# Kernel optimization log

Hardware: AMD Instinct MI355X
Metric: run time of the kernel (lower is better)

Reference implementation:

```python
import jax, jax.numpy as jnp
import numpy as np
from jax import lax

B, T, S, H, E, V = 32, 64, 64, 512, 512, 32000


def setup_inputs() -> dict:
    key = jax.random.key(0)
    ks = jax.random.split(key, 10)
    s = 0.02
    return {
        "sequence": jax.random.randint(ks[0], (B, T), 0, V),
        "encoder_outputs": jax.random.normal(ks[1], (S, B, H), jnp.float32),
        "encoder_hidden": jax.random.normal(ks[2], (B, H), jnp.float32),
        "encoder_cell": jax.random.normal(ks[3], (B, H), jnp.float32),
        "embedding": jax.random.normal(ks[4], (V, E), jnp.float32) * s,
        "W_ih": jax.random.normal(ks[5], (4 * H, E + H), jnp.float32) * s,
        "b_ih": jnp.zeros((4 * H,), jnp.float32),
        "W_hh": jax.random.normal(ks[6], (4 * H, H), jnp.float32) * s,
        "b_hh": jnp.zeros((4 * H,), jnp.float32),
        "W_in_proj": jax.random.normal(ks[7], (H, H), jnp.float32) * s,
        "b_in_proj": jnp.zeros((H,), jnp.float32),
        "W_out_proj": jax.random.normal(ks[8], (H, 2 * H), jnp.float32) * s,
        "b_out_proj": jnp.zeros((H,), jnp.float32),
        "W_final": jax.random.normal(ks[9], (V, H), jnp.float32) * s,
        "b_final": jnp.zeros((V,), jnp.float32),
    }


def reference(sequence, encoder_outputs, encoder_hidden, encoder_cell,
              embedding, W_ih, b_ih, W_hh, b_hh,
              W_in_proj, b_in_proj, W_out_proj, b_out_proj,
              W_final, b_final):
    # embed: [B,T,E] -> [T,B,E] (dropout_in = 0 -> identity)
    x = embedding[sequence].transpose(1, 0, 2)
    input_feed = jnp.zeros((B, H), x.dtype)

    def step(carry, x_t):
        h, c, feed = carry
        inp = jnp.concatenate([x_t, feed], axis=1)          # [B, E+H]
        gates = inp @ W_ih.T + b_ih + h @ W_hh.T + b_hh     # [B, 4H]
        i, f, g, o = jnp.split(gates, 4, axis=1)
        c = jax.nn.sigmoid(f) * c + jax.nn.sigmoid(i) * jnp.tanh(g)
        h = jax.nn.sigmoid(o) * jnp.tanh(c)
        # attention layer (scores computed but unused downstream, as in source)
        xp = h @ W_in_proj.T + b_in_proj                    # [B, H]
        scores = jax.nn.softmax(
            jnp.einsum('sbh,bh->sb', encoder_outputs, xp), axis=0)  # [S, B]
        out = jnp.tanh(jnp.concatenate([xp, h], axis=1) @ W_out_proj.T + b_out_proj)
        return (h, c, out), (out, scores)

    _, (outs, _attn) = lax.scan(step, (encoder_hidden, encoder_cell, input_feed), x)
    # outs: [T,B,H] -> [B,T,H] -> logits [B,T,V]
    logits = outs.transpose(1, 0, 2) @ W_final.T + b_final
    return logits
```

## Files before the change

### kernel.cpp

```cpp
#include <hip/hip_runtime.h>
#include <hip/hip_bf16.h>

#define BB 32
#define TT 64
#define HH 512
#define EE 512
#define VV 32000

typedef float f32x4 __attribute__((ext_vector_type(4)));
typedef float f32x16 __attribute__((ext_vector_type(16)));
typedef __bf16 bf16x8 __attribute__((ext_vector_type(8)));
typedef unsigned short u16x8 __attribute__((ext_vector_type(8)));

static __device__ __forceinline__ unsigned short f2bf(float f) {
  unsigned int u = __builtin_bit_cast(unsigned int, f);
  u += 0x7fffu + ((u >> 16) & 1u);
  return (unsigned short)(u >> 16);
}

__global__ __launch_bounds__(256) void k_cvt_bf16(const float* __restrict__ in,
                                                  unsigned short* __restrict__ out,
                                                  int n8) {
  int tid = blockIdx.x * 256 + threadIdx.x;
  if (tid >= n8) return;
  int idx = tid * 8;
  float4 a = *(const float4*)(in + idx);
  float4 b = *(const float4*)(in + idx + 4);
  u16x8 o;
  o[0] = f2bf(a.x); o[1] = f2bf(a.y); o[2] = f2bf(a.z); o[3] = f2bf(a.w);
  o[4] = f2bf(b.x); o[5] = f2bf(b.y); o[6] = f2bf(b.z); o[7] = f2bf(b.w);
  *(u16x8*)(out + idx) = o;
}

__global__ __launch_bounds__(256) void k_emb(const int* __restrict__ seq,
                                             const float* __restrict__ emb,
                                             unsigned short* __restrict__ out) {
  int tid = blockIdx.x * 256 + threadIdx.x;
  int idx = tid * 8;
  int m = idx >> 9;
  int e0 = idx & 511;
  int t = m >> 5, b = m & 31;
  int s = seq[b * TT + t];
  const float* src = emb + (size_t)s * EE + e0;
  float4 a = *(const float4*)(src);
  float4 c = *(const float4*)(src + 4);
  u16x8 o;
  o[0] = f2bf(a.x); o[1] = f2bf(a.y); o[2] = f2bf(a.z); o[3] = f2bf(a.w);
  o[4] = f2bf(c.x); o[5] = f2bf(c.y); o[6] = f2bf(c.z); o[7] = f2bf(c.w);
  *(u16x8*)(out + m * EE + e0) = o;
}

__global__ __launch_bounds__(256) void k_weff(const float* __restrict__ W_out,
                                              const float* __restrict__ W_in,
                                              float* __restrict__ W_eff) {
  __shared__ float sa[16][17], sb[16][17];
  const int t16 = threadIdx.x & 15, ty = threadIdx.x >> 4;
  const int i = blockIdx.y * 16 + ty, m = blockIdx.x * 16 + t16;
  float acc = 0.f;
  for (int k0 = 0; k0 < HH; k0 += 16) {
    sa[ty][t16] = W_out[i * 1024 + k0 + t16];
    sb[ty][t16] = W_in[(k0 + ty) * HH + m];
    __syncthreads();
#pragma unroll
    for (int kk = 0; kk < 16; ++kk) acc += sa[ty][kk] * sb[kk][t16];
    __syncthreads();
  }
  W_eff[i * HH + m] = acc + W_out[i * 1024 + HH + m];
}

__global__ __launch_bounds__(256) void k_beff(const float* __restrict__ W_out,
                                              const float* __restrict__ b_in,
                                              const float* __restrict__ b_out,
                                              float* __restrict__ b_eff) {
  int i = blockIdx.x * 256 + threadIdx.x;
  if (i >= HH) return;
  float acc = b_out[i];
  for (int k = 0; k < HH; ++k) acc += W_out[i * 1024 + k] * b_in[k];
  b_eff[i] = acc;
}

__global__ __launch_bounds__(256) void k_gemm(const unsigned short* __restrict__ A, int lda,
                                              const unsigned short* __restrict__ Bm, int ldb,
                                              float* __restrict__ C, int ldc,
                                              const float* __restrict__ bias1,
                                              const float* __restrict__ bias2,
                                              const float* __restrict__ biasR1,
                                              const float* __restrict__ biasR2,
                                              int K, int m_panels) {
  __shared__ unsigned short As[128][40];
  __shared__ unsigned short Bs[128][40];
  const int tx = threadIdx.x;
  const int lane = tx & 63, w = tx >> 6;
  const int wrow = (w >> 1) * 64, wcol = (w & 1) * 64;
  const int l15 = lane & 15, lk = lane >> 4;
  const int nb = gridDim.x;
  const int swz = (blockIdx.x & 7) * (nb >> 3) + (blockIdx.x >> 3);
  const int m0 = (swz % m_panels) * 128, n0 = (swz / m_panels) * 128;
  f32x4 acc[4][4] = {};
  for (int k0 = 0; k0 < K; k0 += 32) {
#pragma unroll
    for (int u = 0; u < 2; ++u) {
      int c = u * 256 + tx;
      int row = c >> 2, cc = (c & 3) * 8;
      *(int4*)(&As[row][cc]) = *(const int4*)(A + (size_t)(m0 + row) * lda + k0 + cc);
      *(int4*)(&Bs[row][cc]) = *(const int4*)(Bm + (size_t)(n0 + row) * ldb + k0 + cc);
    }
    __syncthreads();
    bf16x8 av[4], bv[4];
#pragma unroll
    for (int mi = 0; mi < 4; ++mi)
      av[mi] = __builtin_bit_cast(bf16x8, *(const int4*)(&As[wrow + mi * 16 + l15][lk * 8]));
#pragma unroll
    for (int ni = 0; ni < 4; ++ni)
      bv[ni] = __builtin_bit_cast(bf16x8, *(const int4*)(&Bs[wcol + ni * 16 + l15][lk * 8]));
#pragma unroll
    for (int mi = 0; mi < 4; ++mi)
#pragma unroll
      for (int ni = 0; ni < 4; ++ni)
        acc[mi][ni] = __builtin_amdgcn_mfma_f32_16x16x32_bf16(av[mi], bv[ni], acc[mi][ni], 0, 0, 0);
    __syncthreads();
  }
#pragma unroll
  for (int mi = 0; mi < 4; ++mi) {
#pragma unroll
    for (int ni = 0; ni < 4; ++ni) {
      int row = m0 + wrow + mi * 16 + lk * 4;
      int col = n0 + wcol + ni * 16 + l15;
      float bb = 0.f;
      if (bias1) bb += bias1[col];
      if (bias2) bb += bias2[col];
#pragma unroll
      for (int q = 0; q < 4; ++q) {
        float bR = 0.f;
        if (biasR1) bR += biasR1[row + q];
        if (biasR2) bR += biasR2[row + q];
        C[(size_t)(row + q) * ldc + col] = acc[mi][ni][q] + bb + bR;
      }
    }
  }
}

static __device__ __forceinline__ void gbar(unsigned* __restrict__ bar, unsigned gen) {
  __syncthreads();
  if (threadIdx.x == 0) {
    asm volatile("s_waitcnt vmcnt(0)" ::: "memory");
    __hip_atomic_store(&bar[blockIdx.x], gen, __ATOMIC_RELAXED, __HIP_MEMORY_SCOPE_AGENT);
  }
  if (threadIdx.x < 64) {
    while (__hip_atomic_load(&bar[threadIdx.x], __ATOMIC_RELAXED, __HIP_MEMORY_SCOPE_AGENT) < gen)
      __builtin_amdgcn_s_sleep(1);
  }
  __syncthreads();
  asm volatile("" ::: "memory");
}

__global__ __launch_bounds__(256, 1) void k_recur(
    const float* __restrict__ xprojT,
    const unsigned short* __restrict__ wih_b,
    const unsigned short* __restrict__ whh_b,
    const unsigned short* __restrict__ weff_b,
    const float* __restrict__ b_eff,
    const float* __restrict__ enc_c,
    unsigned short* __restrict__ h_ext,
    unsigned short* __restrict__ outs_ext,
    unsigned* __restrict__ bar)
{
  __shared__ int4 Abuf4[4096];
  __shared__ float red[4][32][32];
  char* Abuf = (char*)Abuf4;

  const int tx = threadIdx.x;
  const int bid = blockIdx.x;
  const int i0 = bid * 8;
  const int w = tx >> 6, l = tx & 63;
  const int jl = l & 31;
  const int kh = (l >> 5) * 8;
  const int u = tx >> 5, b = tx & 31;

  bf16x8 wg[16];
  {
    const int jg = (jl >> 3) * 512 + i0 + (jl & 7);
#pragma unroll
    for (int r = 0; r < 16; ++r) {
      int k0 = (w * 16 + r) * 16 + kh;
      const unsigned short* src = (k0 < 512)
          ? wih_b + (size_t)jg * 1024 + 512 + k0
          : whh_b + (size_t)jg * 512 + (k0 - 512);
      wg[r] = __builtin_bit_cast(bf16x8, *(const int4*)src);
    }
  }
  bf16x8 we[8];
  {
    const int wr = (bid >> 2) * 32 + jl;
#pragma unroll
    for (int r = 0; r < 8; ++r) {
      int k0 = (w * 8 + r) * 16 + kh;
      we[r] = __builtin_bit_cast(bf16x8, *(const int4*)(weff_b + (size_t)wr * 512 + k0));
    }
  }
  float c_reg = enc_c[b * 512 + i0 + u];
  const float be = b_eff[i0 + u];

  auto stage = [&](const unsigned short* __restrict__ src, int half) {
#pragma unroll
    for (int rnd = 0; rnd < 8; ++rnd) {
      int id = rnd * 256 + tx;
      int row = id >> 6, c16 = id & 63;
      int4 v = *(const int4*)(src + (size_t)row * 512 + c16 * 8);
      int byte = (row * 2048 + half * 1024 + c16 * 16) ^ ((row & 7) << 4);
      *(int4*)(Abuf + byte) = v;
    }
  };
  auto afrag = [&](int ktile) -> bf16x8 {
    int byte = (jl * 2048 + ktile * 32 + (l >> 5) * 16) ^ ((jl & 7) << 4);
    return __builtin_bit_cast(bf16x8, *(const int4*)(Abuf + byte));
  };

  stage(outs_ext, 0);
  stage(h_ext, 1);
  __syncthreads();

  unsigned gen = 1;
  for (int t = 0; t < 64; ++t) {
    f32x16 acc = {};
#pragma unroll
    for (int r = 0; r < 16; ++r)
      acc = __builtin_amdgcn_mfma_f32_32x32x16_bf16(wg[r], afrag(w * 16 + r), acc, 0, 0, 0);
#pragma unroll
    for (int reg = 0; reg < 16; ++reg) {
      int row = (reg & 3) + 8 * (reg >> 2) + 4 * (l >> 5);
      red[w][row][jl] = acc[reg];
    }
    __syncthreads();
    {
      float g4[4];
#pragma unroll
      for (int g = 0; g < 4; ++g) {
        float s = red[0][g * 8 + u][b] + red[1][g * 8 + u][b]
                + red[2][g * 8 + u][b] + red[3][g * 8 + u][b];
        s += xprojT[(size_t)(g * 512 + i0 + u) * 2048 + t * 32 + b];
        g4[g] = s;
      }
      float si = 1.f / (1.f + __expf(-g4[0]));
      float sf = 1.f / (1.f + __expf(-g4[1]));
      float so = 1.f / (1.f + __expf(-g4[3]));
      float cn = sf * c_reg + si * tanhf(g4[2]);
      c_reg = cn;
      unsigned hb = f2bf(so * tanhf(cn));
      unsigned other = (unsigned)__shfl_down((int)hb, 32);
      if ((u & 1) == 0) {
        unsigned* h32 = (unsigned*)(h_ext + (size_t)(t + 1) * 16384);
        __hip_atomic_store(&h32[b * 256 + bid * 4 + (u >> 1)], hb | (other << 16),
                           __ATOMIC_RELAXED, __HIP_MEMORY_SCOPE_AGENT);
      }
    }
    gbar(bar, gen++);

    stage(h_ext + (size_t)(t + 1) * 16384, 1);
    __syncthreads();
    f32x16 acc2 = {};
#pragma unroll
    for (int r = 0; r < 8; ++r)
      acc2 = __builtin_amdgcn_mfma_f32_32x32x16_bf16(we[r], afrag(32 + w * 8 + r), acc2, 0, 0, 0);
#pragma unroll
    for (int reg = 0; reg < 16; ++reg) {
      int row = (reg & 3) + 8 * (reg >> 2) + 4 * (l >> 5);
      red[w][row][jl] = acc2[reg];
    }
    __syncthreads();
    {
      int row = (bid & 3) * 8 + u;
      float s = red[0][row][b] + red[1][row][b] + red[2][row][b] + red[3][row][b] + be;
      unsigned ob = f2bf(tanhf(s));
      unsigned other = (unsigned)__shfl_down((int)ob, 32);
      if ((u & 1) == 0) {
        unsigned* o32 = (unsigned*)(outs_ext + (size_t)(t + 1) * 16384);
        __hip_atomic_store(&o32[b * 256 + bid * 4 + (u >> 1)], ob | (other << 16),
                           __ATOMIC_RELAXED, __HIP_MEMORY_SCOPE_AGENT);
      }
    }
    gbar(bar, gen++);

    if (t < 63) {
      stage(outs_ext + (size_t)(t + 1) * 16384, 0);
      __syncthreads();
    }
  }
}

__global__ __launch_bounds__(256) void k_tr(const unsigned short* __restrict__ outs,
                                            unsigned short* __restrict__ abt) {
  int tid = blockIdx.x * 256 + threadIdx.x;
  int idx = tid * 8;
  int m = idx >> 9;
  int h0 = idx & 511;
  int b = m >> 6, t = m & 63;
  *(u16x8*)(abt + m * 512 + h0) =
      *(const u16x8*)(outs + (size_t)(t * 32 + b) * 512 + h0);
}

extern "C" void kernel_launch(void* const* d_in, const int* in_sizes, int n_in,
                              void* d_out, int out_size, void* d_ws, size_t ws_size,
                              hipStream_t stream) {
  const int*   seq      = (const int*)d_in[0];
  const float* enc_h    = (const float*)d_in[2];
  const float* enc_c    = (const float*)d_in[3];
  const float* emb      = (const float*)d_in[4];
  const float* W_ih     = (const float*)d_in[5];
  const float* b_ih     = (const float*)d_in[6];
  const float* W_hh     = (const float*)d_in[7];
  const float* b_hh     = (const float*)d_in[8];
  const float* W_inp    = (const float*)d_in[9];
  const float* b_inp    = (const float*)d_in[10];
  const float* W_outp   = (const float*)d_in[11];
  const float* b_outp   = (const float*)d_in[12];
  const float* W_final  = (const float*)d_in[13];
  const float* b_final  = (const float*)d_in[14];
  float* logits = (float*)d_out;

  char* ws = (char*)d_ws;
  size_t off = 0;
  auto alloc = [&](size_t bytes) {
    char* p = ws + off;
    off += (bytes + 255) & ~(size_t)255;
    return p;
  };
  unsigned short* wih_b  = (unsigned short*)alloc((size_t)2048 * 1024 * 2);
  unsigned short* whh_b  = (unsigned short*)alloc((size_t)2048 * 512 * 2);
  unsigned short* wfin_b = (unsigned short*)alloc((size_t)VV * HH * 2);
  unsigned short* weff_b = (unsigned short*)alloc((size_t)512 * 512 * 2);
  unsigned short* emb_b  = (unsigned short*)alloc((size_t)2048 * 512 * 2);
  float* xprojT = (float*)alloc((size_t)2048 * 2048 * 4);
  float* W_eff  = (float*)alloc((size_t)512 * 512 * 4);
  float* b_eff  = (float*)alloc((size_t)512 * 4);
  unsigned short* h_ext  = (unsigned short*)alloc((size_t)65 * 32 * 512 * 2);
  unsigned short* outs_e = (unsigned short*)alloc((size_t)65 * 32 * 512 * 2);
  unsigned short* abt = (unsigned short*)alloc((size_t)2048 * 512 * 2);
  unsigned* bar = (unsigned*)alloc(4096);

  hipMemsetAsync(bar, 0, 4096, stream);
  hipMemsetAsync(outs_e, 0, (size_t)32 * 512 * 2, stream);

  hipLaunchKernelGGL(k_cvt_bf16, dim3(1024), dim3(256), 0, stream, W_ih, wih_b, 2048 * 1024 / 8);
  hipLaunchKernelGGL(k_cvt_bf16, dim3(512), dim3(256), 0, stream, W_hh, whh_b, 2048 * 512 / 8);
  hipLaunchKernelGGL(k_cvt_bf16, dim3(8000), dim3(256), 0, stream, W_final, wfin_b, VV * HH / 8);
  hipLaunchKernelGGL(k_cvt_bf16, dim3(8), dim3(256), 0, stream, enc_h, h_ext, 32 * 512 / 8);
  hipLaunchKernelGGL(k_emb, dim3(512), dim3(256), 0, stream, seq, emb, emb_b);
  hipLaunchKernelGGL(k_weff, dim3(32, 32), dim3(256), 0, stream, W_outp, W_inp, W_eff);
  hipLaunchKernelGGL(k_cvt_bf16, dim3(128), dim3(256), 0, stream, W_eff, weff_b, 512 * 512 / 8);
  hipLaunchKernelGGL(k_beff, dim3(2), dim3(256), 0, stream, W_outp, b_inp, b_outp, b_eff);

  hipLaunchKernelGGL(k_gemm, dim3(256), dim3(256), 0, stream,
                     wih_b, 1024, emb_b, 512, xprojT, 2048,
                     (const float*)nullptr, (const float*)nullptr, b_ih, b_hh, 512, 16);

  hipLaunchKernelGGL(k_recur, dim3(64), dim3(256), 0, stream,
                     xprojT, wih_b, whh_b, weff_b, b_eff, enc_c,
                     h_ext, outs_e, bar);

  hipLaunchKernelGGL(k_tr, dim3(512), dim3(256), 0, stream, outs_e + 16384, abt);
  hipLaunchKernelGGL(k_gemm, dim3(4000), dim3(256), 0, stream,
                     abt, 512, wfin_b, 512, logits, 32000,
                     b_final, (const float*)nullptr, (const float*)nullptr, (const float*)nullptr, 512, 16);
}
```

Before: 818.1 us.

## Fuse W_final bf16 conversion into GEMM and streamline recurrent barrier publishing

The final-logits GEMM now reads W_final as fp32 and converts it to bf16 while loading tiles, which removes the separate conversion kernel and its intermediate buffer. The recurrent kernel pads the barrier flags to separate cache lines, packs h and output values through shared memory into 64-bit atomic stores, and splits staging so each step loads only the needed half. The xproj load and feed staging are hoisted ahead of the MFMA loop to hide latency. In exchange, the big GEMM reads twice as many bytes for B and repeats the conversion for each M panel.

```diff
diff --git a/kernel.cpp b/kernel.cpp
--- a/kernel.cpp
+++ b/kernel.cpp
@@ -80,7 +80,8 @@
 }
 
 __global__ __launch_bounds__(256) void k_gemm(const unsigned short* __restrict__ A, int lda,
-                                              const unsigned short* __restrict__ Bm, int ldb,
+                                              const unsigned short* __restrict__ Bm,
+                                              const float* __restrict__ BmF, int ldb,
                                               float* __restrict__ C, int ldc,
                                               const float* __restrict__ bias1,
                                               const float* __restrict__ bias2,
@@ -103,7 +104,17 @@
       int c = u * 256 + tx;
       int row = c >> 2, cc = (c & 3) * 8;
       *(int4*)(&As[row][cc]) = *(const int4*)(A + (size_t)(m0 + row) * lda + k0 + cc);
-      *(int4*)(&Bs[row][cc]) = *(const int4*)(Bm + (size_t)(n0 + row) * ldb + k0 + cc);
+      if (BmF) {
+        const float* src = BmF + (size_t)(n0 + row) * ldb + k0 + cc;
+        float4 f0 = *(const float4*)src;
+        float4 f1 = *(const float4*)(src + 4);
+        u16x8 pk;
+        pk[0] = f2bf(f0.x); pk[1] = f2bf(f0.y); pk[2] = f2bf(f0.z); pk[3] = f2bf(f0.w);
+        pk[4] = f2bf(f1.x); pk[5] = f2bf(f1.y); pk[6] = f2bf(f1.z); pk[7] = f2bf(f1.w);
+        *(u16x8*)(&Bs[row][cc]) = pk;
+      } else {
+        *(int4*)(&Bs[row][cc]) = *(const int4*)(Bm + (size_t)(n0 + row) * ldb + k0 + cc);
+      }
     }
     __syncthreads();
     bf16x8 av[4], bv[4];
@@ -144,10 +155,10 @@
   __syncthreads();
   if (threadIdx.x == 0) {
     asm volatile("s_waitcnt vmcnt(0)" ::: "memory");
-    __hip_atomic_store(&bar[blockIdx.x], gen, __ATOMIC_RELAXED, __HIP_MEMORY_SCOPE_AGENT);
+    __hip_atomic_store(&bar[blockIdx.x * 32], gen, __ATOMIC_RELAXED, __HIP_MEMORY_SCOPE_AGENT);
   }
   if (threadIdx.x < 64) {
-    while (__hip_atomic_load(&bar[threadIdx.x], __ATOMIC_RELAXED, __HIP_MEMORY_SCOPE_AGENT) < gen)
+    while (__hip_atomic_load(&bar[threadIdx.x * 32], __ATOMIC_RELAXED, __HIP_MEMORY_SCOPE_AGENT) < gen)
       __builtin_amdgcn_s_sleep(1);
   }
   __syncthreads();
@@ -167,6 +178,7 @@
 {
   __shared__ int4 Abuf4[4096];
   __shared__ float red[4][32][32];
+  __shared__ unsigned short s_pub[32][8];
   char* Abuf = (char*)Abuf4;
 
   const int tx = threadIdx.x;
@@ -201,13 +213,23 @@
   float c_reg = enc_c[b * 512 + i0 + u];
   const float be = b_eff[i0 + u];
 
-  auto stage = [&](const unsigned short* __restrict__ src, int half) {
-#pragma unroll
-    for (int rnd = 0; rnd < 8; ++rnd) {
-      int id = rnd * 256 + tx;
-      int row = id >> 6, c16 = id & 63;
-      int4 v = *(const int4*)(src + (size_t)row * 512 + c16 * 8);
-      int byte = (row * 2048 + half * 1024 + c16 * 16) ^ ((row & 7) << 4);
+  auto stage_feed = [&](const unsigned short* __restrict__ src) {
+#pragma unroll
+    for (int r = 0; r < 16; ++r) {
+      int id = r * 64 + l;
+      int row = id >> 5, c = id & 31;
+      int4 v = *(const int4*)(src + (size_t)row * 512 + w * 256 + c * 8);
+      int byte = (row * 2048 + w * 512 + c * 16) ^ ((row & 7) << 4);
+      *(int4*)(Abuf + byte) = v;
+    }
+  };
+  auto stage_h = [&](const unsigned short* __restrict__ src) {
+#pragma unroll
+    for (int r = 0; r < 8; ++r) {
+      int id = r * 64 + l;
+      int row = id >> 4, c = id & 15;
+      int4 v = *(const int4*)(src + (size_t)row * 512 + w * 128 + c * 8);
+      int byte = (row * 2048 + 1024 + w * 256 + c * 16) ^ ((row & 7) << 4);
       *(int4*)(Abuf + byte) = v;
     }
   };
@@ -216,12 +238,16 @@
     return __builtin_bit_cast(bf16x8, *(const int4*)(Abuf + byte));
   };
 
-  stage(outs_ext, 0);
-  stage(h_ext, 1);
+  stage_h(h_ext);
   __syncthreads();
 
   unsigned gen = 1;
   for (int t = 0; t < 64; ++t) {
+    if (w < 2) stage_feed(outs_ext + (size_t)t * 16384);
+    float xp[4];
+#pragma unroll
+    for (int g = 0; g < 4; ++g)
+      xp[g] = xprojT[(size_t)(g * 512 + i0 + u) * 2048 + t * 32 + b];
     f32x16 acc = {};
 #pragma unroll
     for (int r = 0; r < 16; ++r)
@@ -235,29 +261,27 @@
     {
       float g4[4];
 #pragma unroll
-      for (int g = 0; g < 4; ++g) {
-        float s = red[0][g * 8 + u][b] + red[1][g * 8 + u][b]
-                + red[2][g * 8 + u][b] + red[3][g * 8 + u][b];
-        s += xprojT[(size_t)(g * 512 + i0 + u) * 2048 + t * 32 + b];
-        g4[g] = s;
-      }
+      for (int g = 0; g < 4; ++g)
+        g4[g] = red[0][g * 8 + u][b] + red[1][g * 8 + u][b]
+              + red[2][g * 8 + u][b] + red[3][g * 8 + u][b] + xp[g];
       float si = 1.f / (1.f + __expf(-g4[0]));
       float sf = 1.f / (1.f + __expf(-g4[1]));
       float so = 1.f / (1.f + __expf(-g4[3]));
       float cn = sf * c_reg + si * tanhf(g4[2]);
       c_reg = cn;
-      unsigned hb = f2bf(so * tanhf(cn));
-      unsigned other = (unsigned)__shfl_down((int)hb, 32);
-      if ((u & 1) == 0) {
-        unsigned* h32 = (unsigned*)(h_ext + (size_t)(t + 1) * 16384);
-        __hip_atomic_store(&h32[b * 256 + bid * 4 + (u >> 1)], hb | (other << 16),
-                           __ATOMIC_RELAXED, __HIP_MEMORY_SCOPE_AGENT);
-      }
+      s_pub[b][u] = f2bf(so * tanhf(cn));
+    }
+    __syncthreads();
+    if (tx < 64) {
+      int bb = tx & 31, half = tx >> 5;
+      unsigned long long v = *(const unsigned long long*)(&s_pub[bb][half * 4]);
+      unsigned long long* h64 = (unsigned long long*)(h_ext + (size_t)(t + 1) * 16384);
+      __hip_atomic_store(&h64[bb * 128 + bid * 2 + half], v,
+                         __ATOMIC_RELAXED, __HIP_MEMORY_SCOPE_AGENT);
     }
     gbar(bar, gen++);
 
-    stage(h_ext + (size_t)(t + 1) * 16384, 1);
-    __syncthreads();
+    stage_h(h_ext + (size_t)(t + 1) * 16384);
     f32x16 acc2 = {};
 #pragma unroll
     for (int r = 0; r < 8; ++r)
@@ -271,20 +295,17 @@
     {
       int row = (bid & 3) * 8 + u;
       float s = red[0][row][b] + red[1][row][b] + red[2][row][b] + red[3][row][b] + be;
-      unsigned ob = f2bf(tanhf(s));
-      unsigned other = (unsigned)__shfl_down((int)ob, 32);
-      if ((u & 1) == 0) {
-        unsigned* o32 = (unsigned*)(outs_ext + (size_t)(t + 1) * 16384);
-        __hip_atomic_store(&o32[b * 256 + bid * 4 + (u >> 1)], ob | (other << 16),
-                           __ATOMIC_RELAXED, __HIP_MEMORY_SCOPE_AGENT);
-      }
+      s_pub[b][u] = f2bf(tanhf(s));
+    }
+    __syncthreads();
+    if (tx < 64) {
+      int bb = tx & 31, half = tx >> 5;
+      unsigned long long v = *(const unsigned long long*)(&s_pub[bb][half * 4]);
+      unsigned long long* o64 = (unsigned long long*)(outs_ext + (size_t)(t + 1) * 16384);
+      __hip_atomic_store(&o64[bb * 128 + bid * 2 + half], v,
+                         __ATOMIC_RELAXED, __HIP_MEMORY_SCOPE_AGENT);
     }
     gbar(bar, gen++);
-
-    if (t < 63) {
-      stage(outs_ext + (size_t)(t + 1) * 16384, 0);
-      __syncthreads();
-    }
   }
 }
 
@@ -327,7 +348,6 @@
   };
   unsigned short* wih_b  = (unsigned short*)alloc((size_t)2048 * 1024 * 2);
   unsigned short* whh_b  = (unsigned short*)alloc((size_t)2048 * 512 * 2);
-  unsigned short* wfin_b = (unsigned short*)alloc((size_t)VV * HH * 2);
   unsigned short* weff_b = (unsigned short*)alloc((size_t)512 * 512 * 2);
   unsigned short* emb_b  = (unsigned short*)alloc((size_t)2048 * 512 * 2);
   float* xprojT = (float*)alloc((size_t)2048 * 2048 * 4);
@@ -336,14 +356,13 @@
   unsigned short* h_ext  = (unsigned short*)alloc((size_t)65 * 32 * 512 * 2);
   unsigned short* outs_e = (unsigned short*)alloc((size_t)65 * 32 * 512 * 2);
   unsigned short* abt = (unsigned short*)alloc((size_t)2048 * 512 * 2);
-  unsigned* bar = (unsigned*)alloc(4096);
-
-  hipMemsetAsync(bar, 0, 4096, stream);
+  unsigned* bar = (unsigned*)alloc(8192);
+
+  hipMemsetAsync(bar, 0, 8192, stream);
   hipMemsetAsync(outs_e, 0, (size_t)32 * 512 * 2, stream);
 
   hipLaunchKernelGGL(k_cvt_bf16, dim3(1024), dim3(256), 0, stream, W_ih, wih_b, 2048 * 1024 / 8);
   hipLaunchKernelGGL(k_cvt_bf16, dim3(512), dim3(256), 0, stream, W_hh, whh_b, 2048 * 512 / 8);
-  hipLaunchKernelGGL(k_cvt_bf16, dim3(8000), dim3(256), 0, stream, W_final, wfin_b, VV * HH / 8);
   hipLaunchKernelGGL(k_cvt_bf16, dim3(8), dim3(256), 0, stream, enc_h, h_ext, 32 * 512 / 8);
   hipLaunchKernelGGL(k_emb, dim3(512), dim3(256), 0, stream, seq, emb, emb_b);
   hipLaunchKernelGGL(k_weff, dim3(32, 32), dim3(256), 0, stream, W_outp, W_inp, W_eff);
@@ -351,7 +370,7 @@
   hipLaunchKernelGGL(k_beff, dim3(2), dim3(256), 0, stream, W_outp, b_inp, b_outp, b_eff);
 
   hipLaunchKernelGGL(k_gemm, dim3(256), dim3(256), 0, stream,
-                     wih_b, 1024, emb_b, 512, xprojT, 2048,
+                     wih_b, 1024, emb_b, (const float*)nullptr, 512, xprojT, 2048,
                      (const float*)nullptr, (const float*)nullptr, b_ih, b_hh, 512, 16);
 
   hipLaunchKernelGGL(k_recur, dim3(64), dim3(256), 0, stream,
@@ -360,6 +379,6 @@
 
   hipLaunchKernelGGL(k_tr, dim3(512), dim3(256), 0, stream, outs_e + 16384, abt);
   hipLaunchKernelGGL(k_gemm, dim3(4000), dim3(256), 0, stream,
-                     abt, 512, wfin_b, 512, logits, 32000,
+                     abt, 512, (const unsigned short*)nullptr, W_final, 512, logits, 32000,
                      b_final, (const float*)nullptr, (const float*)nullptr, (const float*)nullptr, 512, 16);
 }
```

Result: slower. 1.023 ms (+25.1%).
